# Kernel tuning notes

Hardware: AMD Instinct MI355X
Metric: run time of the kernel (lower is better)

## Reference

```python
import jax, jax.numpy as jnp
import numpy as np

SR = 24000
N_FFT = 2048
WIN = 960
HOP = 240
NUM_BANDS = 150
HID = 128
OUT = 64
LOG_E_MIN = -18.0  # stands in for trained log_energy_min buffer
LOG_E_MAX = 5.0    # stands in for trained log_energy_max buffer
FREQ_INTERVAL = SR / N_FFT


def _stft_power(x):
    # torchaudio Spectrogram(power=2, center=True, pad_mode=reflect)
    pad = N_FFT // 2
    xp = jnp.pad(x, ((0, 0), (pad, pad)), mode='reflect')
    n = jnp.arange(WIN, dtype=jnp.float32)
    win = 0.5 - 0.5 * jnp.cos(2.0 * jnp.pi * n / WIN)  # periodic hann
    lp = (N_FFT - WIN) // 2
    win = jnp.pad(win, (lp, N_FFT - WIN - lp))  # center-pad window to n_fft
    T = 1 + x.shape[1] // HOP
    idx = (jnp.arange(T) * HOP)[:, None] + jnp.arange(N_FFT)[None, :]  # [T, n_fft]
    frames = xp[:, idx] * win  # [B, T, n_fft]
    F = jnp.fft.rfft(frames, axis=-1)  # [B, T, n_fft//2+1]
    return F.real ** 2 + F.imag ** 2


def _lstm_dir(feat_tbd, w_ih, w_hh, b, reverse):
    # feat_tbd: [T, B, D]; PyTorch gate order i, f, g, o
    xs = jnp.flip(feat_tbd, 0) if reverse else feat_tbd
    pre = jnp.einsum('tbd,gd->tbg', xs, w_ih) + b  # input projection hoisted out of scan

    def step(carry, z_in):
        h, c = carry
        z = z_in + h @ w_hh.T
        i, f, g, o = jnp.split(z, 4, axis=-1)
        c = jax.nn.sigmoid(f) * c + jax.nn.sigmoid(i) * jnp.tanh(g)
        h = jax.nn.sigmoid(o) * jnp.tanh(c)
        return (h, c), h

    B = feat_tbd.shape[1]
    h0 = jnp.zeros((B, HID), feat_tbd.dtype)
    _, hs = jax.lax.scan(step, (h0, h0), pre)
    return jnp.flip(hs, 0) if reverse else hs


def setup_inputs() -> dict:
    key = jax.random.key(0)
    ks = jax.random.split(key, 12)
    B, L, T = 16, 240000, 1001
    x = jax.random.normal(ks[0], (B, L), jnp.float32) * 0.1
    f0_raw = jax.random.uniform(ks[1], (B, T), jnp.float32, 50.0, 400.0)
    voiced = jax.random.uniform(ks[2], (B, T)) > 0.1
    f0 = jnp.where(voiced, f0_raw, 0.0)
    D_in = NUM_BANDS * 2 + 1  # 301
    s = 0.08
    return {
        'x': x,
        'f0': f0,
        'w_ih_f': jax.random.normal(ks[3], (4 * HID, D_in), jnp.float32) * s,
        'w_hh_f': jax.random.normal(ks[4], (4 * HID, HID), jnp.float32) * s,
        'b_f': jax.random.normal(ks[5], (4 * HID,), jnp.float32) * s,
        'w_ih_b': jax.random.normal(ks[6], (4 * HID, D_in), jnp.float32) * s,
        'w_hh_b': jax.random.normal(ks[7], (4 * HID, HID), jnp.float32) * s,
        'b_b': jax.random.normal(ks[8], (4 * HID,), jnp.float32) * s,
        'ln_g': jnp.ones((2 * HID,), jnp.float32),
        'ln_b': jnp.zeros((2 * HID,), jnp.float32),
        'out_w': jax.random.normal(ks[9], (OUT, 2 * HID), jnp.float32) * 0.02,
        'out_b': jnp.zeros((OUT,), jnp.float32),
    }


def reference(x, f0, w_ih_f, w_hh_f, b_f, w_ih_b, w_hh_b, b_b, ln_g, ln_b, out_w, out_b):
    spec = _stft_power(x)                     # [B, T, 1025]
    spec = spec.at[..., -1].set(0.0)          # spec[..., -1] = 0
    Tf = min(spec.shape[1], f0.shape[1])
    spec = spec[:, :Tf]
    f0 = f0[:, :Tf]
    f0_nonzero = jnp.where(f0 > 0, f0, SR / NUM_BANDS * 0.5)
    mult = jnp.arange(1.0, NUM_BANDS + 0.5, 0.5, dtype=jnp.float32)  # [299]
    harms = f0_nonzero[..., None] * mult                              # [B, T, 299]
    harms = jnp.concatenate([harms[..., :1] * 0.5, harms], axis=-1)   # [B, T, 300]
    hidx = jnp.clip(jnp.round(harms / FREQ_INTERVAL).astype(jnp.int32), 0, spec.shape[-1] - 1)
    harms_energy = jnp.take_along_axis(spec, hidx, axis=-1)           # irregular gather
    log_energy = jnp.log(harms_energy + 1e-8)
    feature = (log_energy - LOG_E_MIN) / (LOG_E_MAX - LOG_E_MIN)
    feature = jnp.concatenate([feature, jnp.log(f0_nonzero)[..., None]], axis=-1)  # [B, T, 301]
    ft = feature.transpose(1, 0, 2)  # [T, B, 301]
    hf = _lstm_dir(ft, w_ih_f, w_hh_f, b_f, False)
    hb = _lstm_dir(ft, w_ih_b, w_hh_b, b_b, True)
    h = jnp.concatenate([hf, hb], axis=-1).transpose(1, 0, 2)  # [B, T, 256]
    mu = h.mean(-1, keepdims=True)
    var = h.var(-1, keepdims=True)
    hn = (h - mu) / jnp.sqrt(var + 1e-5) * ln_g + ln_b
    return hn @ out_w.T + out_b  # [B, T, 64]
```

## Files before the change

### kernel.cpp

```cpp
#include <hip/hip_runtime.h>

typedef __bf16 bf16x8 __attribute__((ext_vector_type(8)));
typedef float f32x4 __attribute__((ext_vector_type(4)));
typedef int   i32x4 __attribute__((ext_vector_type(4)));

__device__ __forceinline__ void sync_lds() {
    asm volatile("s_waitcnt lgkmcnt(0)" ::: "memory");
    __builtin_amdgcn_s_barrier();
}

__global__ __launch_bounds__(256) void prep_kernel(
    const float* __restrict__ x, const float* __restrict__ w_ih_f, const float* __restrict__ w_ih_b,
    __bf16* __restrict__ BT, __bf16* __restrict__ A, __bf16* __restrict__ WT)
{
    int blk = blockIdx.x;
    if (blk < 7680) {
        int id = blk * 256 + threadIdx.x;
        int n = id / 960;
        int j = id - n * 960;
        int k = n >> 1;
        int p = (k * (544 + j)) & 2047;
        float pr = (float)p * (1.0f / 2048.0f);
        float v = (n & 1) ? __builtin_amdgcn_sinf(pr) : __builtin_amdgcn_cosf(pr);
        BT[id] = (__bf16)v;
    } else if (blk < 37920) {
        int id = (blk - 7680) * 256 + threadIdx.x;
        int frame = id / 480;
        int jp = (id - frame * 480) * 2;
        float v[2] = {0.f, 0.f};
        if (frame < 16016) {
            int b = frame / 1001;
            int t = frame - b * 1001;
            const float* xb = x + (size_t)b * 240000;
            #pragma unroll
            for (int e = 0; e < 2; ++e) {
                int j = jp + e;
                int s = t * 240 + j - 480;
                if (s < 0) s = -s;
                else if (s >= 240000) s = 479998 - s;
                float win = 0.5f - 0.5f * __builtin_amdgcn_cosf((float)j * (1.0f / 960.0f));
                v[e] = xb[s] * win;
            }
        }
        union { unsigned int u; __bf16 h[2]; } pk;
        pk.h[0] = (__bf16)v[0]; pk.h[1] = (__bf16)v[1];
        *reinterpret_cast<unsigned int*>(&A[(size_t)frame * 960 + jp]) = pk.u;
    } else {
        int id = (blk - 37920) * 256 + threadIdx.x;
        int n = id / 320;
        int k = id - n * 320;
        float v = 0.f;
        if (k < 301) v = (n < 512) ? w_ih_f[n * 301 + k] : w_ih_b[(n - 512) * 301 + k];
        WT[id] = (__bf16)v;
    }
}

__global__ __launch_bounds__(256) void gemm_kernel(
    const __bf16* __restrict__ A, const __bf16* __restrict__ BT,
    int Ka, int kIters, int mode,
    __bf16* __restrict__ Cdft, float* __restrict__ pre,
    const float* __restrict__ b_f, const float* __restrict__ b_b)
{
    __shared__ __bf16 As[128 * 64];
    __shared__ __bf16 Bs[128 * 64];
    const int tid = threadIdx.x;
    const int wave = tid >> 6, lane = tid & 63, l15 = lane & 15, quad = lane >> 4;
    const int bn = blockIdx.x, bm = blockIdx.y;
    const int qm = wave >> 1, qn = wave & 1;
    f32x4 acc[4][4] = {};
    const int rl  = lane >> 3;
    const int gch = (lane & 7) ^ rl;
    const __bf16* Ag = A + (size_t)(bm * 128) * Ka;
    const __bf16* Bg = BT + (size_t)(bn * 128) * Ka;

    for (int kb = 0; kb < kIters; ++kb) {
        int k0 = kb * 64;
        #pragma unroll
        for (int p = 0; p < 4; ++p) {
            int c = wave + p * 4;
            int row = c * 8 + rl;
            __builtin_amdgcn_global_load_lds(
                (const __attribute__((address_space(1))) void*)(Ag + (size_t)row * Ka + k0 + gch * 8),
                (__attribute__((address_space(3))) void*)(As + c * 512), 16, 0, 0);
            __builtin_amdgcn_global_load_lds(
                (const __attribute__((address_space(1))) void*)(Bg + (size_t)row * Ka + k0 + gch * 8),
                (__attribute__((address_space(3))) void*)(Bs + c * 512), 16, 0, 0);
        }
        __syncthreads();
        #pragma unroll
        for (int ks = 0; ks < 2; ++ks) {
            bf16x8 af[4], bfr[4];
            #pragma unroll
            for (int i = 0; i < 4; ++i) {
                int row = qm * 64 + i * 16 + l15;
                int ch = (ks * 4 + quad) ^ (l15 & 7);
                af[i] = *reinterpret_cast<const bf16x8*>(&As[row * 64 + ch * 8]);
            }
            #pragma unroll
            for (int j = 0; j < 4; ++j) {
                int row = qn * 64 + j * 16 + l15;
                int ch = (ks * 4 + quad) ^ (l15 & 7);
                bfr[j] = *reinterpret_cast<const bf16x8*>(&Bs[row * 64 + ch * 8]);
            }
            #pragma unroll
            for (int i = 0; i < 4; ++i)
                #pragma unroll
                for (int j = 0; j < 4; ++j)
                    acc[i][j] = __builtin_amdgcn_mfma_f32_16x16x32_bf16(af[i], bfr[j], acc[i][j], 0, 0, 0);
        }
        __syncthreads();
    }

    if (mode == 0) {
        #pragma unroll
        for (int i = 0; i < 4; ++i)
            #pragma unroll
            for (int j = 0; j < 4; ++j) {
                int n = bn * 128 + qn * 64 + j * 16 + l15;
                #pragma unroll
                for (int r = 0; r < 4; ++r) {
                    int m = bm * 128 + qm * 64 + i * 16 + quad * 4 + r;
                    Cdft[(size_t)m * 2048 + n] = (__bf16)acc[i][j][r];
                }
            }
    } else {
        for (int i = 0; i < 4; ++i)
            for (int j = 0; j < 4; ++j) {
                int n = bn * 128 + qn * 64 + j * 16 + l15;
                float bias = (n < 512) ? b_f[n] : b_b[n - 512];
                int dirg = n >> 9;
                int ngate = n & 511;
                int g = ngate >> 7;
                int jj = ngate & 127;
                for (int r = 0; r < 4; ++r) {
                    int m = bm * 128 + qm * 64 + i * 16 + quad * 4 + r;
                    if (m < 16016) {
                        int b = m / 1001;
                        int t = m - b * 1001;
                        size_t off = ((size_t)(t * 2 + dirg) * 16 + b) * 512 + jj * 4 + g;
                        pre[off] = acc[i][j][r] + bias;
                    }
                }
            }
    }
}

__global__ __launch_bounds__(256) void build_feat(const float* __restrict__ f0,
    const __bf16* __restrict__ Cdft, __bf16* __restrict__ feat)
{
    __shared__ __bf16 row[2048];
    const int frame = blockIdx.x;
    const int tid = threadIdx.x;
    __builtin_amdgcn_global_load_lds(
        (const __attribute__((address_space(1))) void*)(Cdft + (size_t)frame * 2048 + tid * 8),
        (__attribute__((address_space(3))) void*)(row + (tid >> 6) * 512), 16, 0, 0);

    int b = frame / 1001;
    int t = frame - b * 1001;
    float f0v = f0[b * 1001 + t];
    float f0nz = (f0v > 0.f) ? f0v : 80.f;
    __syncthreads();

    const float LN2 = 0.6931471805599453f;
    for (int d = tid; d < 320; d += 256) {
        float val = 0.f;
        if (d < 300) {
            float mult = (d == 0) ? 0.5f : (float)(d + 1) * 0.5f;
            int kidx = (int)rintf(f0nz * mult * (1.0f / 11.71875f));
            kidx = min(max(kidx, 0), 1024);
            float e = 0.f;
            if (kidx < 1024) {
                union { unsigned int u; __bf16 h[2]; } c;
                c.u = *reinterpret_cast<const unsigned int*>(&row[2 * kidx]);
                float c0 = (float)c.h[0], c1 = (float)c.h[1];
                e = c0 * c0 + c1 * c1;
            }
            val = (__builtin_amdgcn_logf(e + 1e-8f) * LN2 + 18.f) * (1.f / 23.f);
        } else if (d == 300) {
            val = __builtin_amdgcn_logf(f0nz) * LN2;
        }
        feat[(size_t)frame * 320 + d] = (__bf16)val;
    }
}

__global__ __launch_bounds__(512, 2) void lstm_kernel(
    const float* __restrict__ w_hh_f, const float* __restrict__ w_hh_b,
    const float* __restrict__ pre, float* __restrict__ h_out)
{
    const int bid = blockIdx.x;
    const int b   = bid & 15;
    const int dir = bid >> 4;
    const float* w_hh = dir ? w_hh_b : w_hh_f;
    const int tid = threadIdx.x;
    const int wave = tid >> 6, lane = tid & 63, l15 = lane & 15, quad = lane >> 4;
    const int msel = l15 >> 2;
    const bool own = (quad == (l15 & 3));
    const int cellj = wave * 16 + l15;

    __shared__ __attribute__((aligned(16))) signed char h8[2][128];

    i32x4 afrag[4][2];
    #pragma unroll
    for (int mt = 0; mt < 4; ++mt) {
        int s = wave * 64 + mt * 16 + l15;
        const float* wrow = w_hh + (size_t)((s & 3) * 128 + (s >> 2)) * 128;
        #pragma unroll
        for (int kt = 0; kt < 2; ++kt) {
            i32x4 v;
            #pragma unroll
            for (int d = 0; d < 4; ++d) {
                int pk = 0;
                #pragma unroll
                for (int bi = 0; bi < 4; ++bi) {
                    int k = kt * 64 + quad * 16 + d * 4 + bi;
                    int q = (int)rintf(wrow[k] * 254.f);
                    pk |= (q & 255) << (bi * 8);
                }
                v[d] = pk;
            }
            afrag[mt][kt] = v;
        }
    }

    if (tid < 64) reinterpret_cast<int*>(h8)[tid] = 0;

    const int t0 = dir ? 1000 : 0;
    const ptrdiff_t pre_sstride  = dir ? -16384 : 16384;
    const ptrdiff_t hout_sstride = dir ? -2048  : 2048;
    const float* pre_base = pre + ((size_t)(t0 * 2 + dir) * 16 + b) * 512 + (size_t)cellj * 4;
    float* hout_base = h_out + (((size_t)dir * 1001 + t0) * 16 + b) * 128;

    float cstate = 0.f;
    const float L2E = 1.4426950408889634f;
    const float DF = 1.0f / (254.f * 127.f);

    auto body = [&](int s, f32x4 P) {
        const signed char* hb = h8[s & 1];
        i32x4 b0 = *reinterpret_cast<const i32x4*>(&hb[quad * 16]);
        i32x4 b1 = *reinterpret_cast<const i32x4*>(&hb[64 + quad * 16]);

        i32x4 acc[4] = {};
        #pragma unroll
        for (int mt = 0; mt < 4; ++mt)
            acc[mt] = __builtin_amdgcn_mfma_i32_16x16x64_i8(afrag[mt][0], b0, acc[mt], 0, 0, 0);
        #pragma unroll
        for (int mt = 0; mt < 4; ++mt)
            acc[mt] = __builtin_amdgcn_mfma_i32_16x16x64_i8(afrag[mt][1], b1, acc[mt], 0, 0, 0);

        i32x4 t01 = (msel & 1) ? acc[1] : acc[0];
        i32x4 t23 = (msel & 1) ? acc[3] : acc[2];
        i32x4 z4  = (msel & 2) ? t23 : t01;

        float zi = (float)z4[0] * DF + P[0], zf = (float)z4[1] * DF + P[1];
        float zg = (float)z4[2] * DF + P[2], zo = (float)z4[3] * DF + P[3];
        float A = __builtin_amdgcn_exp2f(-L2E * zi);
        float B = __builtin_amdgcn_exp2f(-L2E * zf);
        float C = __builtin_amdgcn_exp2f(-2.f * L2E * zg);
        float D = __builtin_amdgcn_exp2f(-L2E * zo);
        float Pp = (1.f + A) * (1.f + C);
        float Q = 1.f + B;
        float cn = (cstate * Pp + (1.f - C) * Q) * __builtin_amdgcn_rcpf(Pp * Q);
        if (own) cstate = cn;
        float E = __builtin_amdgcn_exp2f(-2.f * L2E * cn);
        float h = (1.f - E) * __builtin_amdgcn_rcpf((1.f + D) * (1.f + E));

        if (own) {
            h8[(s + 1) & 1][cellj] = (signed char)(int)rintf(h * 127.f);
            hout_base[(ptrdiff_t)s * hout_sstride + cellj] = h;
        }
    };

    auto load_pre = [&](int sidx) -> f32x4 {
        return *reinterpret_cast<const f32x4*>(pre_base + (ptrdiff_t)sidx * pre_sstride);
    };

    f32x4 PA = load_pre(0);
    f32x4 PB = load_pre(1);
    __syncthreads();

    for (int s = 0; s < 1001; s += 2) {
        body(s, PA);
        PA = load_pre(s + 2);
        sync_lds();
        if (s + 1 < 1001) {
            body(s + 1, PB);
            PB = load_pre(s + 3);
            sync_lds();
        }
    }
}

__global__ __launch_bounds__(256) void out_kernel(
    const float* __restrict__ h_out, const float* __restrict__ ln_g, const float* __restrict__ ln_b,
    const float* __restrict__ out_w, const float* __restrict__ out_b, float* __restrict__ out)
{
    __shared__ __bf16 hn_lds[16 * 264];
    const int tid = threadIdx.x;
    const int wave = tid >> 6, lane = tid & 63, l15 = lane & 15, quad = lane >> 4;

    float lg0 = ln_g[lane],        lb0 = ln_b[lane];
    float lg1 = ln_g[64 + lane],   lb1 = ln_b[64 + lane];
    float lg2 = ln_g[128 + lane],  lb2 = ln_b[128 + lane];
    float lg3 = ln_g[192 + lane],  lb3 = ln_b[192 + lane];

    #pragma unroll
    for (int rr = 0; rr < 4; ++rr) {
        int wrow = wave * 4 + rr;
        int r = blockIdx.x * 16 + wrow;
        int b = r / 1001, t = r - b * 1001;
        size_t basef = ((size_t)t * 16 + b) * 128;
        size_t baseb = ((size_t)(1001 + t) * 16 + b) * 128;
        float h0 = h_out[basef + lane];
        float h1 = h_out[basef + 64 + lane];
        float h2 = h_out[baseb + lane];
        float h3 = h_out[baseb + 64 + lane];
        float s1 = h0 + h1 + h2 + h3;
        float s2 = h0 * h0 + h1 * h1 + h2 * h2 + h3 * h3;
        #pragma unroll
        for (int m = 32; m >= 1; m >>= 1) {
            s1 += __shfl_xor(s1, m, 64);
            s2 += __shfl_xor(s2, m, 64);
        }
        float mu = s1 * (1.f / 256.f);
        float var = s2 * (1.f / 256.f) - mu * mu;
        float rstd = rsqrtf(var + 1e-5f);
        hn_lds[wrow * 264 + lane]       = (__bf16)((h0 - mu) * rstd * lg0 + lb0);
        hn_lds[wrow * 264 + 64 + lane]  = (__bf16)((h1 - mu) * rstd * lg1 + lb1);
        hn_lds[wrow * 264 + 128 + lane] = (__bf16)((h2 - mu) * rstd * lg2 + lb2);
        hn_lds[wrow * 264 + 192 + lane] = (__bf16)((h3 - mu) * rstd * lg3 + lb3);
    }
    __syncthreads();

    const int o = wave * 16 + l15;
    f32x4 accA = {}, accB = {};
    #pragma unroll
    for (int kt = 0; kt < 8; ++kt) {
        bf16x8 a = *reinterpret_cast<const bf16x8*>(&hn_lds[l15 * 264 + kt * 32 + quad * 8]);
        const float* wp = out_w + (size_t)o * 256 + kt * 32 + quad * 8;
        bf16x8 bv;
        #pragma unroll
        for (int e = 0; e < 8; ++e) bv[e] = (__bf16)wp[e];
        if (kt & 1) accB = __builtin_amdgcn_mfma_f32_16x16x32_bf16(a, bv, accB, 0, 0, 0);
        else        accA = __builtin_amdgcn_mfma_f32_16x16x32_bf16(a, bv, accA, 0, 0, 0);
    }
    f32x4 acc = accA + accB;
    float ob = out_b[o];
    #pragma unroll
    for (int rc = 0; rc < 4; ++rc) {
        int r = blockIdx.x * 16 + quad * 4 + rc;
        out[(size_t)r * 64 + o] = acc[rc] + ob;
    }
}

extern "C" void kernel_launch(void* const* d_in, const int* in_sizes, int n_in,
                              void* d_out, int out_size, void* d_ws, size_t ws_size,
                              hipStream_t stream) {
    const float* x      = (const float*)d_in[0];
    const float* f0     = (const float*)d_in[1];
    const float* w_ih_f = (const float*)d_in[2];
    const float* w_hh_f = (const float*)d_in[3];
    const float* b_f    = (const float*)d_in[4];
    const float* w_ih_b = (const float*)d_in[5];
    const float* w_hh_b = (const float*)d_in[6];
    const float* b_b    = (const float*)d_in[7];
    const float* ln_g   = (const float*)d_in[8];
    const float* ln_b   = (const float*)d_in[9];
    const float* out_w  = (const float*)d_in[10];
    const float* out_b  = (const float*)d_in[11];
    float* out = (float*)d_out;

    char* ws = (char*)d_ws;
    size_t off = 0;
    auto alloc = [&](size_t bytes) { size_t o = off; off = (off + bytes + 255) & ~(size_t)255; return o; };
    __bf16* A     = (__bf16*)(ws + alloc((size_t)16128 * 960 * 2));
    __bf16* BT    = (__bf16*)(ws + alloc((size_t)2048 * 960 * 2));
    __bf16* Cdft  = (__bf16*)(ws + alloc((size_t)16128 * 2048 * 2));
    __bf16* feat  = (__bf16*)(ws + alloc((size_t)16128 * 320 * 2));
    __bf16* WT    = (__bf16*)(ws + alloc((size_t)1024 * 320 * 2));
    float*  preA  = (float*)(ws + alloc((size_t)(1001 * 2 + 8) * 16 * 512 * 4));
    float*  pre   = preA + (size_t)4 * 16 * 512;
    float*  h_out = (float*)(ws + alloc((size_t)2 * 1001 * 16 * 128 * 4));
    (void)ws_size; (void)in_sizes; (void)n_in; (void)out_size;

    prep_kernel <<<39200, 256, 0, stream>>>(x, w_ih_f, w_ih_b, BT, A, WT);
    gemm_kernel <<<dim3(16, 126), 256, 0, stream>>>(A, BT, 960, 15, 0, Cdft, nullptr, nullptr, nullptr);
    build_feat  <<<16016, 256, 0, stream>>>(f0, Cdft, feat);
    gemm_kernel <<<dim3(8, 126), 256, 0, stream>>>(feat, WT, 320, 5, 1, nullptr, pre, b_f, b_b);
    lstm_kernel <<<32, 512, 0, stream>>>(w_hh_f, w_hh_b, pre, h_out);
    out_kernel  <<<1001, 256, 0, stream>>>(h_out, ln_g, ln_b, out_w, out_b, out);
}
```

Before: 636.2 us.

## Halve LSTM block to 4 waves with 8 MFMA tiles per wave, prescale gates

```diff
diff --git a/kernel.cpp b/kernel.cpp
--- a/kernel.cpp
+++ b/kernel.cpp
@@ -124,6 +124,7 @@
                 }
             }
     } else {
+        const float L2E = 1.4426950408889634f;
         for (int i = 0; i < 4; ++i)
             for (int j = 0; j < 4; ++j) {
                 int n = bn * 128 + qn * 64 + j * 16 + l15;
@@ -132,13 +133,14 @@
                 int ngate = n & 511;
                 int g = ngate >> 7;
                 int jj = ngate & 127;
+                float gam = (g == 2) ? (-2.f * L2E) : (-L2E);
                 for (int r = 0; r < 4; ++r) {
                     int m = bm * 128 + qm * 64 + i * 16 + quad * 4 + r;
                     if (m < 16016) {
                         int b = m / 1001;
                         int t = m - b * 1001;
                         size_t off = ((size_t)(t * 2 + dirg) * 16 + b) * 512 + jj * 4 + g;
-                        pre[off] = acc[i][j][r] + bias;
+                        pre[off] = gam * (acc[i][j][r] + bias);
                     }
                 }
             }
@@ -183,7 +185,7 @@
     }
 }
 
-__global__ __launch_bounds__(512, 2) void lstm_kernel(
+__global__ __launch_bounds__(256) void lstm_kernel(
     const float* __restrict__ w_hh_f, const float* __restrict__ w_hh_b,
     const float* __restrict__ pre, float* __restrict__ h_out)
 {
@@ -193,16 +195,16 @@
     const float* w_hh = dir ? w_hh_b : w_hh_f;
     const int tid = threadIdx.x;
     const int wave = tid >> 6, lane = tid & 63, l15 = lane & 15, quad = lane >> 4;
-    const int msel = l15 >> 2;
-    const bool own = (quad == (l15 & 3));
-    const int cellj = wave * 16 + l15;
+    const bool own = ((l15 & 1) == 0);
+    const int cellj = wave * 32 + ((l15 >> 1) << 2) + quad;
+    const int m0 = (l15 >> 1) & 1, m1 = (l15 >> 2) & 1, m2 = (l15 >> 3) & 1;
 
     __shared__ __attribute__((aligned(16))) signed char h8[2][128];
 
-    i32x4 afrag[4][2];
+    i32x4 afrag[8][2];
     #pragma unroll
-    for (int mt = 0; mt < 4; ++mt) {
-        int s = wave * 64 + mt * 16 + l15;
+    for (int mt = 0; mt < 8; ++mt) {
+        int s = wave * 128 + mt * 16 + l15;
         const float* wrow = w_hh + (size_t)((s & 3) * 128 + (s >> 2)) * 128;
         #pragma unroll
         for (int kt = 0; kt < 2; ++kt) {
@@ -228,45 +230,53 @@
     const ptrdiff_t pre_sstride  = dir ? -16384 : 16384;
     const ptrdiff_t hout_sstride = dir ? -2048  : 2048;
     const float* pre_base = pre + ((size_t)(t0 * 2 + dir) * 16 + b) * 512 + (size_t)cellj * 4;
-    float* hout_base = h_out + (((size_t)dir * 1001 + t0) * 16 + b) * 128;
+    float* hout_base = h_out + (((size_t)dir * 1001 + t0) * 16 + b) * 128 + cellj;
 
     float cstate = 0.f;
     const float L2E = 1.4426950408889634f;
     const float DF = 1.0f / (254.f * 127.f);
+    const float CI = -L2E * DF;
+    const float CG = -2.f * L2E * DF;
 
     auto body = [&](int s, f32x4 P) {
         const signed char* hb = h8[s & 1];
         i32x4 b0 = *reinterpret_cast<const i32x4*>(&hb[quad * 16]);
         i32x4 b1 = *reinterpret_cast<const i32x4*>(&hb[64 + quad * 16]);
 
-        i32x4 acc[4] = {};
-        #pragma unroll
-        for (int mt = 0; mt < 4; ++mt)
+        i32x4 acc[8] = {};
+        #pragma unroll
+        for (int mt = 0; mt < 8; ++mt)
             acc[mt] = __builtin_amdgcn_mfma_i32_16x16x64_i8(afrag[mt][0], b0, acc[mt], 0, 0, 0);
         #pragma unroll
-        for (int mt = 0; mt < 4; ++mt)
+        for (int mt = 0; mt < 8; ++mt)
             acc[mt] = __builtin_amdgcn_mfma_i32_16x16x64_i8(afrag[mt][1], b1, acc[mt], 0, 0, 0);
 
-        i32x4 t01 = (msel & 1) ? acc[1] : acc[0];
-        i32x4 t23 = (msel & 1) ? acc[3] : acc[2];
-        i32x4 z4  = (msel & 2) ? t23 : t01;
-
-        float zi = (float)z4[0] * DF + P[0], zf = (float)z4[1] * DF + P[1];
-        float zg = (float)z4[2] * DF + P[2], zo = (float)z4[3] * DF + P[3];
-        float A = __builtin_amdgcn_exp2f(-L2E * zi);
-        float B = __builtin_amdgcn_exp2f(-L2E * zf);
-        float C = __builtin_amdgcn_exp2f(-2.f * L2E * zg);
-        float D = __builtin_amdgcn_exp2f(-L2E * zo);
+        i32x4 ta = m0 ? acc[1] : acc[0];
+        i32x4 tb = m0 ? acc[3] : acc[2];
+        i32x4 tc = m0 ? acc[5] : acc[4];
+        i32x4 td = m0 ? acc[7] : acc[6];
+        i32x4 ua = m1 ? tb : ta;
+        i32x4 ub = m1 ? td : tc;
+        i32x4 z4 = m2 ? ub : ua;
+
+        float ai = fmaf((float)z4[0], CI, P[0]);
+        float af_ = fmaf((float)z4[1], CI, P[1]);
+        float ag = fmaf((float)z4[2], CG, P[2]);
+        float ao = fmaf((float)z4[3], CI, P[3]);
+        float A = __builtin_amdgcn_exp2f(ai);
+        float B = __builtin_amdgcn_exp2f(af_);
+        float C = __builtin_amdgcn_exp2f(ag);
+        float D = __builtin_amdgcn_exp2f(ao);
         float Pp = (1.f + A) * (1.f + C);
         float Q = 1.f + B;
         float cn = (cstate * Pp + (1.f - C) * Q) * __builtin_amdgcn_rcpf(Pp * Q);
-        if (own) cstate = cn;
+        cstate = cn;
         float E = __builtin_amdgcn_exp2f(-2.f * L2E * cn);
         float h = (1.f - E) * __builtin_amdgcn_rcpf((1.f + D) * (1.f + E));
 
         if (own) {
             h8[(s + 1) & 1][cellj] = (signed char)(int)rintf(h * 127.f);
-            hout_base[(ptrdiff_t)s * hout_sstride + cellj] = h;
+            hout_base[(ptrdiff_t)s * hout_sstride] = h;
         }
     };
 
@@ -274,20 +284,16 @@
         return *reinterpret_cast<const f32x4*>(pre_base + (ptrdiff_t)sidx * pre_sstride);
     };
 
-    f32x4 PA = load_pre(0);
-    f32x4 PB = load_pre(1);
+    f32x4 P0 = load_pre(0), P1 = load_pre(1), P2 = load_pre(2), P3 = load_pre(3);
     __syncthreads();
 
-    for (int s = 0; s < 1001; s += 2) {
-        body(s, PA);
-        PA = load_pre(s + 2);
-        sync_lds();
-        if (s + 1 < 1001) {
-            body(s + 1, PB);
-            PB = load_pre(s + 3);
-            sync_lds();
-        }
-    }
+    for (int s = 0; s < 1000; s += 4) {
+        body(s, P0);     P0 = load_pre(s + 4); sync_lds();
+        body(s + 1, P1); P1 = load_pre(s + 5); sync_lds();
+        body(s + 2, P2); P2 = load_pre(s + 6); sync_lds();
+        body(s + 3, P3); P3 = load_pre(s + 7); sync_lds();
+    }
+    body(1000, P0);
 }
 
 __global__ __launch_bounds__(256) void out_kernel(
@@ -377,8 +383,8 @@
     __bf16* Cdft  = (__bf16*)(ws + alloc((size_t)16128 * 2048 * 2));
     __bf16* feat  = (__bf16*)(ws + alloc((size_t)16128 * 320 * 2));
     __bf16* WT    = (__bf16*)(ws + alloc((size_t)1024 * 320 * 2));
-    float*  preA  = (float*)(ws + alloc((size_t)(1001 * 2 + 8) * 16 * 512 * 4));
-    float*  pre   = preA + (size_t)4 * 16 * 512;
+    float*  preA  = (float*)(ws + alloc((size_t)(1001 * 2 + 16) * 16 * 512 * 4));
+    float*  pre   = preA + (size_t)8 * 16 * 512;
     float*  h_out = (float*)(ws + alloc((size_t)2 * 1001 * 16 * 128 * 4));
     (void)ws_size; (void)in_sizes; (void)n_in; (void)out_size;
 
@@ -386,6 +392,6 @@
     gemm_kernel <<<dim3(16, 126), 256, 0, stream>>>(A, BT, 960, 15, 0, Cdft, nullptr, nullptr, nullptr);
     build_feat  <<<16016, 256, 0, stream>>>(f0, Cdft, feat);
     gemm_kernel <<<dim3(8, 126), 256, 0, stream>>>(feat, WT, 320, 5, 1, nullptr, pre, b_f, b_b);
-    lstm_kernel <<<32, 512, 0, stream>>>(w_hh_f, w_hh_b, pre, h_out);
+    lstm_kernel <<<32, 256, 0, stream>>>(w_hh_f, w_hh_b, pre, h_out);
     out_kernel  <<<1001, 256, 0, stream>>>(h_out, ln_g, ln_b, out_w, out_b, out);
 }
```

Measured after the change: 618.3 us. 1.03x faster.
